# Kernel tuning notes

Hardware: AMD Instinct MI355X
Metric: run time of the kernel (lower is better)

Reference implementation:

```python
import jax, jax.numpy as jnp
import numpy as np

D_MODEL = 1024
N_HEADS = 16
D_HEAD = D_MODEL // N_HEADS
LORA_RANK = 8
LORA_ALPHA = 16
LORA_SCALING = LORA_ALPHA / LORA_RANK
NEG_INF = -1.0e9


def setup_inputs() -> dict:
    key = jax.random.key(0)
    ks = jax.random.split(key, 8)
    B, S = 2, 2048
    s_in = 1.0 / np.sqrt(D_MODEL)
    return {
        "x": jax.random.normal(ks[0], (B, S, D_MODEL), dtype=jnp.float32),
        "attention_mask": jnp.ones((B, S), dtype=jnp.int32),
        "W_qkv_kernel": jax.random.normal(ks[1], (D_MODEL, 3 * D_MODEL), jnp.float32) * s_in,
        "W_qkv_bias": jnp.zeros((3 * D_MODEL,), jnp.float32),
        "lora_A_qkv": jax.random.normal(ks[2], (D_MODEL, LORA_RANK), jnp.float32) * 0.01,
        "lora_B_qkv": jax.random.normal(ks[3], (LORA_RANK, 3 * D_MODEL), jnp.float32) * 0.01,
        "c_proj_kernel": jax.random.normal(ks[4], (D_MODEL, D_MODEL), jnp.float32) * s_in,
        "c_proj_bias": jnp.zeros((D_MODEL,), jnp.float32),
        "lora_A_proj": jax.random.normal(ks[5], (D_MODEL, LORA_RANK), jnp.float32) * 0.01,
        "lora_B_proj": jax.random.normal(ks[6], (LORA_RANK, D_MODEL), jnp.float32) * 0.01,
    }


def reference(x, attention_mask, W_qkv_kernel, W_qkv_bias, lora_A_qkv, lora_B_qkv,
              c_proj_kernel, c_proj_bias, lora_A_proj, lora_B_proj):
    B, S, _ = x.shape
    # QKV projection + LoRA adapter
    qkv = x @ W_qkv_kernel + W_qkv_bias
    qkv = qkv + ((x @ lora_A_qkv) @ lora_B_qkv) * LORA_SCALING
    q, k, v = jnp.split(qkv, 3, axis=-1)
    # [B, H, S, Dh]
    q = q.reshape(B, S, N_HEADS, D_HEAD).transpose(0, 2, 1, 3)
    k = k.reshape(B, S, N_HEADS, D_HEAD).transpose(0, 2, 1, 3)
    v = v.reshape(B, S, N_HEADS, D_HEAD).transpose(0, 2, 1, 3)
    # raw scores [B, H, S, S]
    scores = jnp.einsum("bhqd,bhkd->bhqk", q, k)
    # padding mask applied BEFORE scaling (as in the original)
    pad = (attention_mask[:, None, None, :] == 0)
    scores = jnp.where(pad, NEG_INF, scores)
    # causal mask (lower triangular kept)
    causal = jnp.tril(jnp.ones((S, S), dtype=bool))
    scores = jnp.where(causal[None, None, :, :], scores, NEG_INF)
    # scaling applied AFTER masking (faithful to source: -1e9 also divided)
    scaled = scores / jnp.sqrt(jnp.float32(D_HEAD))
    attn = jax.nn.softmax(scaled, axis=-1)
    ctx = jnp.einsum("bhqk,bhkd->bhqd", attn, v)
    ctx = ctx.transpose(0, 2, 1, 3).reshape(B, S, D_MODEL)
    out = ctx @ c_proj_kernel + c_proj_bias
    out = out + ((ctx @ lora_A_proj) @ lora_B_proj) * LORA_SCALING
    return out
```

## Files before the change

### kernel.cpp

```cpp
#include <hip/hip_runtime.h>
#include <hip/hip_bf16.h>

#define LOG2E 1.4426950408889634f
#define MASKVAL (-1.25e8f * LOG2E)

typedef __bf16 bf16x8 __attribute__((ext_vector_type(8)));
typedef __bf16 bf16x4 __attribute__((ext_vector_type(4)));
typedef short  shortx4 __attribute__((ext_vector_type(4)));
typedef float  floatx4 __attribute__((ext_vector_type(4)));

__device__ __forceinline__ floatx4 mfma16(bf16x8 a, bf16x8 b, floatx4 c) {
  return __builtin_amdgcn_mfma_f32_16x16x32_bf16(a, b, c, 0, 0, 0);
}

__device__ __forceinline__ floatx4 mfma_pv(bf16x4 a, bf16x4 b, floatx4 c) {
#if __has_builtin(__builtin_amdgcn_mfma_f32_16x16x16_bf16)
  return __builtin_amdgcn_mfma_f32_16x16x16_bf16(a, b, c, 0, 0, 0);
#else
  shortx4 as, bs;
  __builtin_memcpy(&as, &a, 8);
  __builtin_memcpy(&bs, &b, 8);
  return __builtin_amdgcn_mfma_f32_16x16x16bf16_1k(as, bs, c, 0, 0, 0);
#endif
}

__device__ __forceinline__ void load_lds16(const __bf16* g, __bf16* l) {
  __builtin_amdgcn_global_load_lds(
      (const __attribute__((address_space(1))) void*)g,
      (__attribute__((address_space(3))) void*)l, 16, 0, 0);
}

__device__ __forceinline__ float max3f(float a, float b, float c) {
  return fmaxf(a, fmaxf(b, c));
}

__global__ __launch_bounds__(256)
void fold_wt2(const float* __restrict__ Wq, const float* __restrict__ Aq,
              const float* __restrict__ Bq, __bf16* __restrict__ WTq,
              const float* __restrict__ Wp, const float* __restrict__ Ap,
              const float* __restrict__ Bp, __bf16* __restrict__ WTp) {
  __shared__ float tile[64][65];
  __shared__ float sLb[8][64];
  const int bx = blockIdx.x;
  const bool isQ = bx < 48;
  const float* W  = isQ ? Wq : Wp;
  const float* La = isQ ? Aq : Ap;
  const float* Lb = isQ ? Bq : Bp;
  __bf16* WT = isQ ? WTq : WTp;
  const int ncols = isQ ? 3072 : 1024;
  const int nt = (isQ ? bx : bx - 48) * 64;
  const int kt = blockIdx.y * 64;
  const int tid = threadIdx.x;
  const int tx = tid & 63, ty = tid >> 6;

  float rLa[8];
  *(float4*)&rLa[0] = *(const float4*)(La + (size_t)(kt + tx) * 8);
  *(float4*)&rLa[4] = *(const float4*)(La + (size_t)(kt + tx) * 8 + 4);

#pragma unroll
  for (int rep = 0; rep < 2; rep++) {
    int idx = tid + rep * 256;
    sLb[idx >> 6][idx & 63] = Lb[(size_t)(idx >> 6) * ncols + nt + (idx & 63)];
  }
#pragma unroll
  for (int rep = 0; rep < 16; rep++) {
    int i = rep * 4 + ty;
    tile[i][tx] = W[(size_t)(kt + i) * ncols + nt + tx];
  }
  __syncthreads();
#pragma unroll
  for (int rep = 0; rep < 16; rep++) {
    int i = rep * 4 + ty;
    int n = nt + i, k = kt + tx;
    float acc = tile[tx][i];
#pragma unroll
    for (int r = 0; r < 8; r++)
      acc += 2.0f * rLa[r] * sLb[r][i];
    WT[(size_t)n * 1024 + k] = (__bf16)acc;
  }
}

__global__ __launch_bounds__(256)
void cast_x(const float* __restrict__ x, __bf16* __restrict__ o) {
  int i = blockIdx.x * 256 + threadIdx.x;
  float4 v = ((const float4*)x)[i];
  bf16x4 r = {(__bf16)v.x, (__bf16)v.y, (__bf16)v.z, (__bf16)v.w};
  ((bf16x4*)o)[i] = r;
}

__global__ __launch_bounds__(256)
void gemm_qkv(const __bf16* __restrict__ WT, const __bf16* __restrict__ X,
              const float* __restrict__ bias, __bf16* __restrict__ qk,
              __bf16* __restrict__ vtb) {
  const int K = 1024;
  __shared__ alignas(16) __bf16 smem[32768];
  const int tid = threadIdx.x;
  const int wave = tid >> 6, lane = tid & 63;
  const int wm = wave >> 1, wn = wave & 1;
  const int quad = lane >> 4, l15 = lane & 15;
  const int p0 = blockIdx.y * 128, s0 = blockIdx.x * 128;
  const int srow8 = lane >> 3, sc8 = lane & 7;
  const int sswz = sc8 ^ srow8;

  auto STAGE = [&](int bb, int kb) {
    __bf16* Ab = smem + bb * 8192;
    __bf16* Bb = smem + 16384 + bb * 8192;
#pragma unroll
    for (int t = 0; t < 4; t++) {
      int rbase = (wave * 4 + t) * 8;
      int row = rbase + srow8;
      load_lds16(WT + (size_t)(p0 + row) * K + kb + sswz * 8, Ab + rbase * 64);
      load_lds16(X + (size_t)(s0 + row) * K + kb + sswz * 8, Bb + rbase * 64);
    }
  };

  floatx4 acc[4][4] = {};
  STAGE(0, 0);

  for (int it = 0; it < 16; it++) {
    const int cur = it & 1;
    if (it < 15) {
      STAGE(cur ^ 1, (it + 1) * 64);
      asm volatile("s_waitcnt vmcnt(8)" ::: "memory");
    } else {
      asm volatile("s_waitcnt vmcnt(0)" ::: "memory");
    }
    __builtin_amdgcn_s_barrier();
    __builtin_amdgcn_sched_barrier(0);
    const __bf16* Ac = smem + cur * 8192;
    const __bf16* Bc = smem + 16384 + cur * 8192;
#pragma unroll
    for (int ks = 0; ks < 2; ks++) {
      bf16x8 af[4], bfv[4];
#pragma unroll
      for (int t = 0; t < 4; t++) {
        int ra = wm * 64 + t * 16 + l15;
        int rb = wn * 64 + t * 16 + l15;
        int ch = (ks * 4 + quad) ^ (l15 & 7);
        af[t]  = *(const bf16x8*)(Ac + ra * 64 + ch * 8);
        bfv[t] = *(const bf16x8*)(Bc + rb * 64 + ch * 8);
      }
#pragma unroll
      for (int mi = 0; mi < 4; mi++)
#pragma unroll
        for (int ni = 0; ni < 4; ni++)
          acc[mi][ni] = mfma16(af[mi], bfv[ni], acc[mi][ni]);
    }
    __builtin_amdgcn_s_barrier();
  }

  __bf16* ep = smem;
  const int b = s0 >> 11, s2b = s0 & 2047;

  if (p0 < 2048) {
    const float qscale = (p0 < 1024) ? 0.125f * LOG2E : 1.0f;
#pragma unroll
    for (int mi = 0; mi < 4; mi++) {
      int ch0 = wm * 64 + mi * 16 + quad * 4;
      float4 b4 = *(const float4*)(bias + p0 + ch0);
#pragma unroll
      for (int ni = 0; ni < 4; ni++) {
        int tl = wn * 64 + ni * 16 + l15;
        bf16x4 o = {(__bf16)((acc[mi][ni][0] + b4.x) * qscale),
                    (__bf16)((acc[mi][ni][1] + b4.y) * qscale),
                    (__bf16)((acc[mi][ni][2] + b4.z) * qscale),
                    (__bf16)((acc[mi][ni][3] + b4.w) * qscale)};
        *(bf16x4*)(ep + tl * 136 + ch0) = o;
      }
    }
    __syncthreads();
    const int part = p0 >> 10;
    const int h0 = (p0 & 1023) >> 6;
    const int hs = wave & 1, tb = (wave >> 1) * 64;
    __bf16* outp = qk + (size_t)part * 4194304 +
                   ((size_t)((b * 16 + h0 + hs) * 2048 + s2b)) * 64;
#pragma unroll
    for (int j = 0; j < 8; j++) {
      int tok = tb + j * 8 + (lane >> 3);
      int dh = (lane & 7) * 8;
      bf16x8 v = *(const bf16x8*)(ep + tok * 136 + hs * 64 + dh);
      *(bf16x8*)(outp + (size_t)tok * 64 + dh) = v;
    }
  } else {
#pragma unroll
    for (int mi = 0; mi < 4; mi++) {
      int ch0 = wm * 64 + mi * 16 + quad * 4;
      float4 b4 = *(const float4*)(bias + p0 + ch0);
#pragma unroll
      for (int ni = 0; ni < 4; ni++) {
        int tl = wn * 64 + ni * 16 + l15;
        int off = tl & 63, t = off >> 4, qd = (off >> 2) & 3, rr = off & 3;
        int ptl = (tl & 64) | ((t >> 1) * 32 + qd * 8 + (t & 1) * 4 + rr);
        ep[(ch0 + 0) * 136 + ptl] = (__bf16)(acc[mi][ni][0] + b4.x);
        ep[(ch0 + 1) * 136 + ptl] = (__bf16)(acc[mi][ni][1] + b4.y);
        ep[(ch0 + 2) * 136 + ptl] = (__bf16)(acc[mi][ni][2] + b4.z);
        ep[(ch0 + 3) * 136 + ptl] = (__bf16)(acc[mi][ni][3] + b4.w);
      }
    }
    __syncthreads();
    const int h0 = (p0 & 1023) >> 6;
#pragma unroll
    for (int j = 0; j < 8; j++) {
      int ch = wave * 32 + j * 4 + (lane >> 4);
      int to = (lane & 15) * 8;
      bf16x8 v = *(const bf16x8*)(ep + ch * 136 + to);
      int h = h0 + (ch >> 6), dh = ch & 63;
      *(bf16x8*)(vtb + ((size_t)((b * 16 + h) * 64 + dh)) * 2048 + s2b + to) =
          v;
    }
  }
}

__global__ __launch_bounds__(256)
void gemm_proj(const __bf16* __restrict__ A, const __bf16* __restrict__ BT,
               const float* __restrict__ bias, float* __restrict__ Cout, int N) {
  const int K = 1024;
  __shared__ alignas(16) __bf16 smem[24576];
  const int tid = threadIdx.x;
  const int wave = tid >> 6, lane = tid & 63;
  const int wm = wave >> 1, wn = wave & 1;
  const int quad = lane >> 4, l15 = lane & 15;
  const int m0 = blockIdx.y * 64, n0 = blockIdx.x * 128;
  const int srow8 = lane >> 3, sc8 = lane & 7;
  const int sswz = sc8 ^ srow8;

  auto STAGE = [&](int bb, int kb) {
    __bf16* Ab = smem + bb * 4096;
    __bf16* Bb = smem + 8192 + bb * 8192;
#pragma unroll
    for (int t = 0; t < 2; t++) {
      int rbase = (wave * 2 + t) * 8;
      load_lds16(A + (size_t)(m0 + rbase + srow8) * K + kb + sswz * 8,
                 Ab + rbase * 64);
    }
#pragma unroll
    for (int t = 0; t < 4; t++) {
      int rbase = (wave * 4 + t) * 8;
      load_lds16(BT + (size_t)(n0 + rbase + srow8) * K + kb + sswz * 8,
                 Bb + rbase * 64);
    }
  };

  floatx4 acc[2][4] = {};
  STAGE(0, 0);

  for (int it = 0; it < 16; it++) {
    const int cur = it & 1;
    if (it < 15) {
      STAGE(cur ^ 1, (it + 1) * 64);
      asm volatile("s_waitcnt vmcnt(6)" ::: "memory");
    } else {
      asm volatile("s_waitcnt vmcnt(0)" ::: "memory");
    }
    __builtin_amdgcn_s_barrier();
    __builtin_amdgcn_sched_barrier(0);
    const __bf16* Ac = smem + cur * 4096;
    const __bf16* Bc = smem + 8192 + cur * 8192;
#pragma unroll
    for (int ks = 0; ks < 2; ks++) {
      bf16x8 af[2], bfv[4];
      int ch = (ks * 4 + quad) ^ (l15 & 7);
#pragma unroll
      for (int t = 0; t < 2; t++)
        af[t] = *(const bf16x8*)(Ac + (wm * 32 + t * 16 + l15) * 64 + ch * 8);
#pragma unroll
      for (int t = 0; t < 4; t++)
        bfv[t] = *(const bf16x8*)(Bc + (wn * 64 + t * 16 + l15) * 64 + ch * 8);
#pragma unroll
      for (int mi = 0; mi < 2; mi++)
#pragma unroll
        for (int ni = 0; ni < 4; ni++)
          acc[mi][ni] = mfma16(af[mi], bfv[ni], acc[mi][ni]);
    }
    __builtin_amdgcn_s_barrier();
  }

#pragma unroll
  for (int mi = 0; mi < 2; mi++)
#pragma unroll
    for (int ni = 0; ni < 4; ni++) {
      int n = n0 + wn * 64 + ni * 16 + l15;
#pragma unroll
      for (int r = 0; r < 4; r++) {
        int m = m0 + wm * 32 + mi * 16 + quad * 4 + r;
        Cout[(size_t)m * N + n] = acc[mi][ni][r] + bias[n];
      }
    }
}

__global__ __launch_bounds__(256)
void flash_attn(const __bf16* __restrict__ q, const __bf16* __restrict__ k,
                const __bf16* __restrict__ vt, const int* __restrict__ amask,
                __bf16* __restrict__ ctx) {
  const int S = 2048;
  __shared__ alignas(16) __bf16 Ks[2][64 * 64];
  __shared__ alignas(16) __bf16 Vs[2][64 * 64];
  const int bid = blockIdx.x;
  const int jb = 31 - (bid >> 5);
  const int bh = bid & 31;
  const int b = bh >> 4, h = bh & 15;
  const int wave = threadIdx.x >> 6, lane = threadIdx.x & 63;
  const int quad = lane >> 4, l15 = lane & 15;
  const int srow8 = lane >> 3, sc8 = lane & 7;
  const int sswz = sc8 ^ srow8;
  const int Q0 = jb * 64;
  const int qrow = Q0 + wave * 16 + l15;

  const __bf16* qp  = q  + (size_t)bh * S * 64;
  const __bf16* kp0 = k  + (size_t)bh * S * 64;
  const __bf16* vp0 = vt + (size_t)bh * 64 * S;

  int anyp = 0;
  const int npre = (jb + 4) >> 2;
  for (int it = 0; it < npre; it++) {
    int4 v = *(const int4*)(amask + b * S + it * 256 + lane * 4);
    anyp |= (v.x == 0) | (v.y == 0) | (v.z == 0) | (v.w == 0);
  }
  const bool padded = (__ballot(anyp) != 0ull);

  bf16x8 qf[2];
#pragma unroll
  for (int ks = 0; ks < 2; ks++)
    qf[ks] = *(const bf16x8*)(qp + (size_t)qrow * 64 + ks * 32 + quad * 8);

  auto STAGE = [&](int bb, int cc) {
#pragma unroll
    for (int t = 0; t < 2; t++) {
      int rbase = (wave * 2 + t) * 8;
      load_lds16(kp0 + (size_t)cc * 4096 + (size_t)(rbase + srow8) * 64 +
                     sswz * 8,
                 &Ks[bb][rbase * 64]);
    }
#pragma unroll
    for (int t = 0; t < 2; t++) {
      int rbase = (wave * 2 + t) * 8;
      load_lds16(vp0 + (size_t)(rbase + srow8) * S + cc * 64 + sswz * 8,
                 &Vs[bb][rbase * 64]);
    }
  };

  STAGE(0, 0);

  float mrun = 0.0f, lrun = 0.0f;
  floatx4 oacc[4] = {};

  for (int c = 0; c <= jb; c++) {
    const int cur = c & 1;
    if (c < jb) {
      STAGE(cur ^ 1, c + 1);
      asm volatile("s_waitcnt vmcnt(4)" ::: "memory");
    } else {
      asm volatile("s_waitcnt vmcnt(0)" ::: "memory");
    }
    __builtin_amdgcn_s_barrier();
    __builtin_amdgcn_sched_barrier(0);

    floatx4 st[4] = {};
    __builtin_amdgcn_s_setprio(1);
#pragma unroll
    for (int ks = 0; ks < 2; ks++) {
      const int ch = (ks * 4 + quad) ^ (l15 & 7);
      bf16x8 kf[4];
#pragma unroll
      for (int nt = 0; nt < 4; nt++)
        kf[nt] = *(const bf16x8*)(&Ks[cur][(nt * 16 + l15) * 64 + ch * 8]);
#pragma unroll
      for (int nt = 0; nt < 4; nt++)
        st[nt] = mfma16(kf[nt], qf[ks], st[nt]);
    }
    __builtin_amdgcn_s_setprio(0);

    if (padded) {
      int am_c = amask[b * S + c * 64 + lane];
      unsigned long long pm = __ballot(am_c == 0);
#pragma unroll
      for (int nt = 0; nt < 4; nt++) {
        int kl = nt * 16 + quad * 4;
#pragma unroll
        for (int r = 0; r < 4; r++) {
          bool pad = (pm >> (kl + r)) & 1ull;
          bool masked = pad || ((c == jb) && (kl + r > wave * 16 + l15));
          st[nt][r] = masked ? MASKVAL : st[nt][r];
        }
      }
    } else if (c == jb) {
#pragma unroll
      for (int nt = 0; nt < 4; nt++) {
        int kl = nt * 16 + quad * 4;
#pragma unroll
        for (int r = 0; r < 4; r++) {
          bool masked = kl + r > wave * 16 + l15;
          st[nt][r] = masked ? MASKVAL : st[nt][r];
        }
      }
    }

    float t0 = max3f(st[0][0], st[0][1], st[0][2]);
    float t1 = max3f(st[0][3], st[1][0], st[1][1]);
    float t2 = max3f(st[1][2], st[1][3], st[2][0]);
    float t3 = max3f(st[2][1], st[2][2], st[2][3]);
    float t4 = max3f(st[3][0], st[3][1], st[3][2]);
    float inm = fmaxf(max3f(t0, t1, t2), max3f(t3, t4, st[3][3]));
#pragma unroll
    for (int nt = 0; nt < 4; nt++)
#pragma unroll
      for (int r = 0; r < 4; r++)
        st[nt][r] = exp2f(st[nt][r] - mrun);
    float ssum = (((st[0][0] + st[0][1]) + (st[0][2] + st[0][3])) +
                  ((st[1][0] + st[1][1]) + (st[1][2] + st[1][3]))) +
                 (((st[2][0] + st[2][1]) + (st[2][2] + st[2][3])) +
                  ((st[3][0] + st[3][1]) + (st[3][2] + st[3][3])));
    if (!__all(inm - mrun <= 8.0f)) {
      float rm = fmaxf(inm, __shfl_xor(inm, 16, 64));
      rm = fmaxf(rm, __shfl_xor(rm, 32, 64));
      float mnew = fmaxf(mrun, rm);
      float al = exp2f(mrun - mnew);
      mrun = mnew;
      lrun *= al;
      ssum *= al;
#pragma unroll
      for (int nt = 0; nt < 4; nt++)
#pragma unroll
        for (int r = 0; r < 4; r++) st[nt][r] *= al;
#pragma unroll
      for (int nd = 0; nd < 4; nd++)
#pragma unroll
        for (int r = 0; r < 4; r++) oacc[nd][r] *= al;
    }
    lrun += ssum;

    bf16x4 pB[4];
#pragma unroll
    for (int nt = 0; nt < 4; nt++) {
      bf16x4 pk = {(__bf16)st[nt][0], (__bf16)st[nt][1],
                   (__bf16)st[nt][2], (__bf16)st[nt][3]};
      pB[nt] = pk;
    }

    __builtin_amdgcn_s_setprio(1);
#pragma unroll
    for (int tp = 0; tp < 2; tp++) {
      const int chv = (tp * 4 + quad) ^ (l15 & 7);
#pragma unroll
      for (int nd = 0; nd < 4; nd++) {
        bf16x8 v8 =
            *(const bf16x8*)(&Vs[cur][(nd * 16 + l15) * 64 + chv * 8]);
        bf16x4 vA0 = {v8[0], v8[1], v8[2], v8[3]};
        bf16x4 vA1 = {v8[4], v8[5], v8[6], v8[7]};
        oacc[nd] = mfma_pv(vA0, pB[2 * tp], oacc[nd]);
        oacc[nd] = mfma_pv(vA1, pB[2 * tp + 1], oacc[nd]);
      }
    }
    __builtin_amdgcn_s_setprio(0);

    __builtin_amdgcn_s_barrier();
  }

  lrun += __shfl_xor(lrun, 16, 64);
  lrun += __shfl_xor(lrun, 32, 64);

  const float linv = 1.0f / lrun;
#pragma unroll
  for (int nd = 0; nd < 4; nd++) {
    bf16x4 o = {(__bf16)(oacc[nd][0] * linv), (__bf16)(oacc[nd][1] * linv),
                (__bf16)(oacc[nd][2] * linv), (__bf16)(oacc[nd][3] * linv)};
    *(bf16x4*)(ctx + ((size_t)(b * 2048 + qrow)) * 1024 + h * 64 + nd * 16 +
               quad * 4) = o;
  }
}

extern "C" void kernel_launch(void* const* d_in, const int* in_sizes, int n_in,
                              void* d_out, int out_size, void* d_ws, size_t ws_size,
                              hipStream_t stream) {
  const float* x  = (const float*)d_in[0];
  const int*   am = (const int*)d_in[1];
  const float* Wq = (const float*)d_in[2];
  const float* bq = (const float*)d_in[3];
  const float* Aq = (const float*)d_in[4];
  const float* Bq = (const float*)d_in[5];
  const float* Wp = (const float*)d_in[6];
  const float* bp = (const float*)d_in[7];
  const float* Ap = (const float*)d_in[8];
  const float* Bp = (const float*)d_in[9];

  __bf16* wqkvT = (__bf16*)d_ws;
  __bf16* wpT   = wqkvT + (size_t)3072 * 1024;
  __bf16* xbf   = wpT   + (size_t)1024 * 1024;
  __bf16* qbuf  = xbf   + (size_t)4096 * 1024;
  __bf16* vtbuf = qbuf  + (size_t)2 * 4194304;
  __bf16* ctxb  = vtbuf + (size_t)4194304;

  fold_wt2<<<dim3(64, 16), 256, 0, stream>>>(Wq, Aq, Bq, wqkvT,
                                             Wp, Ap, Bp, wpT);
  cast_x<<<4096, 256, 0, stream>>>(x, xbf);

  gemm_qkv<<<dim3(32, 24), 256, 0, stream>>>(wqkvT, xbf, bq, qbuf, vtbuf);
  flash_attn<<<1024, 256, 0, stream>>>(qbuf, qbuf + 4194304, vtbuf, am, ctxb);
  gemm_proj<<<dim3(8, 64), 256, 0, stream>>>(ctxb, wpT, bp, (float*)d_out, 1024);
}
```

Before: 187.2 us.

## Retile output projection to 128x128 swapped-operand tiles; unroll attention loop by two

The output projection GEMM moves from 64x128 tiles to 128x128 tiles with the weight as the M operand and ctx as N. Each thread can then write contiguous float4 outputs with vectorized bias loads instead of scalar strided stores, and reuse per staged tile goes up, but the grid shrinks to 256 blocks and LDS use grows. Flash attention now calls the raw hardware exp2 builtin instead of exp2f. Its chunk loop is unrolled by two so the double-buffer index is a compile-time constant.

```diff
diff --git a/kernel.cpp b/kernel.cpp
--- a/kernel.cpp
+++ b/kernel.cpp
@@ -32,6 +32,10 @@
 
 __device__ __forceinline__ float max3f(float a, float b, float c) {
   return fmaxf(a, fmaxf(b, c));
+}
+
+__device__ __forceinline__ float exp2r(float x) {
+  return __builtin_amdgcn_exp2f(x);
 }
 
 __global__ __launch_bounds__(256)
@@ -212,62 +216,60 @@
 }
 
 __global__ __launch_bounds__(256)
-void gemm_proj(const __bf16* __restrict__ A, const __bf16* __restrict__ BT,
+void gemm_proj(const __bf16* __restrict__ Actx, const __bf16* __restrict__ BT,
                const float* __restrict__ bias, float* __restrict__ Cout, int N) {
   const int K = 1024;
-  __shared__ alignas(16) __bf16 smem[24576];
+  __shared__ alignas(16) __bf16 smem[32768];
   const int tid = threadIdx.x;
   const int wave = tid >> 6, lane = tid & 63;
   const int wm = wave >> 1, wn = wave & 1;
   const int quad = lane >> 4, l15 = lane & 15;
-  const int m0 = blockIdx.y * 64, n0 = blockIdx.x * 128;
+  const int p0 = blockIdx.y * 128;
+  const int s0 = blockIdx.x * 128;
   const int srow8 = lane >> 3, sc8 = lane & 7;
   const int sswz = sc8 ^ srow8;
 
   auto STAGE = [&](int bb, int kb) {
-    __bf16* Ab = smem + bb * 4096;
-    __bf16* Bb = smem + 8192 + bb * 8192;
-#pragma unroll
-    for (int t = 0; t < 2; t++) {
-      int rbase = (wave * 2 + t) * 8;
-      load_lds16(A + (size_t)(m0 + rbase + srow8) * K + kb + sswz * 8,
-                 Ab + rbase * 64);
-    }
+    __bf16* Ab = smem + bb * 8192;
+    __bf16* Bb = smem + 16384 + bb * 8192;
 #pragma unroll
     for (int t = 0; t < 4; t++) {
       int rbase = (wave * 4 + t) * 8;
-      load_lds16(BT + (size_t)(n0 + rbase + srow8) * K + kb + sswz * 8,
+      int row = rbase + srow8;
+      load_lds16(BT + (size_t)(p0 + row) * K + kb + sswz * 8, Ab + rbase * 64);
+      load_lds16(Actx + (size_t)(s0 + row) * K + kb + sswz * 8,
                  Bb + rbase * 64);
     }
   };
 
-  floatx4 acc[2][4] = {};
+  floatx4 acc[4][4] = {};
   STAGE(0, 0);
 
   for (int it = 0; it < 16; it++) {
     const int cur = it & 1;
     if (it < 15) {
       STAGE(cur ^ 1, (it + 1) * 64);
-      asm volatile("s_waitcnt vmcnt(6)" ::: "memory");
+      asm volatile("s_waitcnt vmcnt(8)" ::: "memory");
     } else {
       asm volatile("s_waitcnt vmcnt(0)" ::: "memory");
     }
     __builtin_amdgcn_s_barrier();
     __builtin_amdgcn_sched_barrier(0);
-    const __bf16* Ac = smem + cur * 4096;
-    const __bf16* Bc = smem + 8192 + cur * 8192;
+    const __bf16* Ac = smem + cur * 8192;
+    const __bf16* Bc = smem + 16384 + cur * 8192;
 #pragma unroll
     for (int ks = 0; ks < 2; ks++) {
-      bf16x8 af[2], bfv[4];
-      int ch = (ks * 4 + quad) ^ (l15 & 7);
-#pragma unroll
-      for (int t = 0; t < 2; t++)
-        af[t] = *(const bf16x8*)(Ac + (wm * 32 + t * 16 + l15) * 64 + ch * 8);
-#pragma unroll
-      for (int t = 0; t < 4; t++)
-        bfv[t] = *(const bf16x8*)(Bc + (wn * 64 + t * 16 + l15) * 64 + ch * 8);
-#pragma unroll
-      for (int mi = 0; mi < 2; mi++)
+      bf16x8 af[4], bfv[4];
+#pragma unroll
+      for (int t = 0; t < 4; t++) {
+        int ra = wm * 64 + t * 16 + l15;
+        int rb = wn * 64 + t * 16 + l15;
+        int ch = (ks * 4 + quad) ^ (l15 & 7);
+        af[t]  = *(const bf16x8*)(Ac + ra * 64 + ch * 8);
+        bfv[t] = *(const bf16x8*)(Bc + rb * 64 + ch * 8);
+      }
+#pragma unroll
+      for (int mi = 0; mi < 4; mi++)
 #pragma unroll
         for (int ni = 0; ni < 4; ni++)
           acc[mi][ni] = mfma16(af[mi], bfv[ni], acc[mi][ni]);
@@ -276,16 +278,17 @@
   }
 
 #pragma unroll
-  for (int mi = 0; mi < 2; mi++)
+  for (int mi = 0; mi < 4; mi++) {
+    int n = p0 + wm * 64 + mi * 16 + quad * 4;
+    float4 b4 = *(const float4*)(bias + n);
 #pragma unroll
     for (int ni = 0; ni < 4; ni++) {
-      int n = n0 + wn * 64 + ni * 16 + l15;
-#pragma unroll
-      for (int r = 0; r < 4; r++) {
-        int m = m0 + wm * 32 + mi * 16 + quad * 4 + r;
-        Cout[(size_t)m * N + n] = acc[mi][ni][r] + bias[n];
-      }
-    }
+      int m = s0 + wn * 64 + ni * 16 + l15;
+      float4 o = {acc[mi][ni][0] + b4.x, acc[mi][ni][1] + b4.y,
+                  acc[mi][ni][2] + b4.z, acc[mi][ni][3] + b4.w};
+      *(float4*)(Cout + (size_t)m * N + n) = o;
+    }
+  }
 }
 
 __global__ __launch_bounds__(256)
@@ -344,8 +347,7 @@
   float mrun = 0.0f, lrun = 0.0f;
   floatx4 oacc[4] = {};
 
-  for (int c = 0; c <= jb; c++) {
-    const int cur = c & 1;
+  auto CHUNK = [&](int c, int cur) {
     if (c < jb) {
       STAGE(cur ^ 1, c + 1);
       asm volatile("s_waitcnt vmcnt(4)" ::: "memory");
@@ -405,7 +407,7 @@
     for (int nt = 0; nt < 4; nt++)
 #pragma unroll
       for (int r = 0; r < 4; r++)
-        st[nt][r] = exp2f(st[nt][r] - mrun);
+        st[nt][r] = exp2r(st[nt][r] - mrun);
     float ssum = (((st[0][0] + st[0][1]) + (st[0][2] + st[0][3])) +
                   ((st[1][0] + st[1][1]) + (st[1][2] + st[1][3]))) +
                  (((st[2][0] + st[2][1]) + (st[2][2] + st[2][3])) +
@@ -414,7 +416,7 @@
       float rm = fmaxf(inm, __shfl_xor(inm, 16, 64));
       rm = fmaxf(rm, __shfl_xor(rm, 32, 64));
       float mnew = fmaxf(mrun, rm);
-      float al = exp2f(mrun - mnew);
+      float al = exp2r(mrun - mnew);
       mrun = mnew;
       lrun *= al;
       ssum *= al;
@@ -454,6 +456,11 @@
     __builtin_amdgcn_s_setprio(0);
 
     __builtin_amdgcn_s_barrier();
+  };
+
+  for (int c = 0; c <= jb; c += 2) {
+    CHUNK(c, 0);
+    if (c + 1 <= jb) CHUNK(c + 1, 1);
   }
 
   lrun += __shfl_xor(lrun, 16, 64);
@@ -496,5 +503,5 @@
 
   gemm_qkv<<<dim3(32, 24), 256, 0, stream>>>(wqkvT, xbf, bq, qbuf, vtbuf);
   flash_attn<<<1024, 256, 0, stream>>>(qbuf, qbuf + 4194304, vtbuf, am, ctxb);
-  gemm_proj<<<dim3(8, 64), 256, 0, stream>>>(ctxb, wpT, bp, (float*)d_out, 1024);
-}
+  gemm_proj<<<dim3(32, 8), 256, 0, stream>>>(ctxb, wpT, bp, (float*)d_out, 1024);
+}
```

After: 179.6 us. -4.1%, faster.

## Merge fold and cast kernels, transpose proj GEMM tiles, use raw exp2, unroll attention loop

Applied to the files above, without the earlier changes.

Merges the weight-fold and x-cast kernels into one launch, which removes a kernel launch. It swaps the operand roles in the output projection GEMM so each thread can write float4 stores with a vectorized bias load. The flash-attention loop is unrolled by two with a constant double-buffer index, and exp2f is replaced by the hardware exp2 intrinsic. The raw exp2 may differ slightly in denormal or accuracy handling.

```diff
diff --git a/kernel.cpp b/kernel.cpp
--- a/kernel.cpp
+++ b/kernel.cpp
@@ -34,14 +34,28 @@
   return fmaxf(a, fmaxf(b, c));
 }
 
+__device__ __forceinline__ float exp2r(float x) {
+  return __builtin_amdgcn_exp2f(x);
+}
+
 __global__ __launch_bounds__(256)
-void fold_wt2(const float* __restrict__ Wq, const float* __restrict__ Aq,
-              const float* __restrict__ Bq, __bf16* __restrict__ WTq,
-              const float* __restrict__ Wp, const float* __restrict__ Ap,
-              const float* __restrict__ Bp, __bf16* __restrict__ WTp) {
+void fold_cast(const float* __restrict__ Wq, const float* __restrict__ Aq,
+               const float* __restrict__ Bq, __bf16* __restrict__ WTq,
+               const float* __restrict__ Wp, const float* __restrict__ Ap,
+               const float* __restrict__ Bp, __bf16* __restrict__ WTp,
+               const float* __restrict__ x, __bf16* __restrict__ xo) {
+  const int bid = blockIdx.x;
+  const int tid = threadIdx.x;
+  if (bid >= 1024) {
+    int i = (bid - 1024) * 256 + tid;
+    float4 v = ((const float4*)x)[i];
+    bf16x4 r = {(__bf16)v.x, (__bf16)v.y, (__bf16)v.z, (__bf16)v.w};
+    ((bf16x4*)xo)[i] = r;
+    return;
+  }
   __shared__ float tile[64][65];
   __shared__ float sLb[8][64];
-  const int bx = blockIdx.x;
+  const int bx = bid & 63;
   const bool isQ = bx < 48;
   const float* W  = isQ ? Wq : Wp;
   const float* La = isQ ? Aq : Ap;
@@ -49,8 +63,7 @@
   __bf16* WT = isQ ? WTq : WTp;
   const int ncols = isQ ? 3072 : 1024;
   const int nt = (isQ ? bx : bx - 48) * 64;
-  const int kt = blockIdx.y * 64;
-  const int tid = threadIdx.x;
+  const int kt = (bid >> 6) * 64;
   const int tx = tid & 63, ty = tid >> 6;
 
   float rLa[8];
@@ -78,14 +91,6 @@
       acc += 2.0f * rLa[r] * sLb[r][i];
     WT[(size_t)n * 1024 + k] = (__bf16)acc;
   }
-}
-
-__global__ __launch_bounds__(256)
-void cast_x(const float* __restrict__ x, __bf16* __restrict__ o) {
-  int i = blockIdx.x * 256 + threadIdx.x;
-  float4 v = ((const float4*)x)[i];
-  bf16x4 r = {(__bf16)v.x, (__bf16)v.y, (__bf16)v.z, (__bf16)v.w};
-  ((bf16x4*)o)[i] = r;
 }
 
 __global__ __launch_bounds__(256)
@@ -212,7 +217,7 @@
 }
 
 __global__ __launch_bounds__(256)
-void gemm_proj(const __bf16* __restrict__ A, const __bf16* __restrict__ BT,
+void gemm_proj(const __bf16* __restrict__ Actx, const __bf16* __restrict__ BT,
                const float* __restrict__ bias, float* __restrict__ Cout, int N) {
   const int K = 1024;
   __shared__ alignas(16) __bf16 smem[24576];
@@ -220,7 +225,8 @@
   const int wave = tid >> 6, lane = tid & 63;
   const int wm = wave >> 1, wn = wave & 1;
   const int quad = lane >> 4, l15 = lane & 15;
-  const int m0 = blockIdx.y * 64, n0 = blockIdx.x * 128;
+  const int p0 = blockIdx.y * 64;
+  const int s0 = blockIdx.x * 128;
   const int srow8 = lane >> 3, sc8 = lane & 7;
   const int sswz = sc8 ^ srow8;
 
@@ -230,13 +236,13 @@
 #pragma unroll
     for (int t = 0; t < 2; t++) {
       int rbase = (wave * 2 + t) * 8;
-      load_lds16(A + (size_t)(m0 + rbase + srow8) * K + kb + sswz * 8,
+      load_lds16(BT + (size_t)(p0 + rbase + srow8) * K + kb + sswz * 8,
                  Ab + rbase * 64);
     }
 #pragma unroll
     for (int t = 0; t < 4; t++) {
       int rbase = (wave * 4 + t) * 8;
-      load_lds16(BT + (size_t)(n0 + rbase + srow8) * K + kb + sswz * 8,
+      load_lds16(Actx + (size_t)(s0 + rbase + srow8) * K + kb + sswz * 8,
                  Bb + rbase * 64);
     }
   };
@@ -276,16 +282,17 @@
   }
 
 #pragma unroll
-  for (int mi = 0; mi < 2; mi++)
+  for (int mi = 0; mi < 2; mi++) {
+    int n = p0 + wm * 32 + mi * 16 + quad * 4;
+    float4 b4 = *(const float4*)(bias + n);
 #pragma unroll
     for (int ni = 0; ni < 4; ni++) {
-      int n = n0 + wn * 64 + ni * 16 + l15;
-#pragma unroll
-      for (int r = 0; r < 4; r++) {
-        int m = m0 + wm * 32 + mi * 16 + quad * 4 + r;
-        Cout[(size_t)m * N + n] = acc[mi][ni][r] + bias[n];
-      }
-    }
+      int m = s0 + wn * 64 + ni * 16 + l15;
+      float4 o = {acc[mi][ni][0] + b4.x, acc[mi][ni][1] + b4.y,
+                  acc[mi][ni][2] + b4.z, acc[mi][ni][3] + b4.w};
+      *(float4*)(Cout + (size_t)m * N + n) = o;
+    }
+  }
 }
 
 __global__ __launch_bounds__(256)
@@ -344,8 +351,7 @@
   float mrun = 0.0f, lrun = 0.0f;
   floatx4 oacc[4] = {};
 
-  for (int c = 0; c <= jb; c++) {
-    const int cur = c & 1;
+  auto CHUNK = [&](int c, int cur) {
     if (c < jb) {
       STAGE(cur ^ 1, c + 1);
       asm volatile("s_waitcnt vmcnt(4)" ::: "memory");
@@ -405,7 +411,7 @@
     for (int nt = 0; nt < 4; nt++)
 #pragma unroll
       for (int r = 0; r < 4; r++)
-        st[nt][r] = exp2f(st[nt][r] - mrun);
+        st[nt][r] = exp2r(st[nt][r] - mrun);
     float ssum = (((st[0][0] + st[0][1]) + (st[0][2] + st[0][3])) +
                   ((st[1][0] + st[1][1]) + (st[1][2] + st[1][3]))) +
                  (((st[2][0] + st[2][1]) + (st[2][2] + st[2][3])) +
@@ -414,7 +420,7 @@
       float rm = fmaxf(inm, __shfl_xor(inm, 16, 64));
       rm = fmaxf(rm, __shfl_xor(rm, 32, 64));
       float mnew = fmaxf(mrun, rm);
-      float al = exp2f(mrun - mnew);
+      float al = exp2r(mrun - mnew);
       mrun = mnew;
       lrun *= al;
       ssum *= al;
@@ -454,6 +460,11 @@
     __builtin_amdgcn_s_setprio(0);
 
     __builtin_amdgcn_s_barrier();
+  };
+
+  for (int c = 0; c <= jb; c += 2) {
+    CHUNK(c, 0);
+    if (c + 1 <= jb) CHUNK(c + 1, 1);
   }
 
   lrun += __shfl_xor(lrun, 16, 64);
@@ -490,11 +501,10 @@
   __bf16* vtbuf = qbuf  + (size_t)2 * 4194304;
   __bf16* ctxb  = vtbuf + (size_t)4194304;
 
-  fold_wt2<<<dim3(64, 16), 256, 0, stream>>>(Wq, Aq, Bq, wqkvT,
-                                             Wp, Ap, Bp, wpT);
-  cast_x<<<4096, 256, 0, stream>>>(x, xbf);
+  fold_cast<<<5120, 256, 0, stream>>>(Wq, Aq, Bq, wqkvT, Wp, Ap, Bp, wpT,
+                                      x, xbf);
 
   gemm_qkv<<<dim3(32, 24), 256, 0, stream>>>(wqkvT, xbf, bq, qbuf, vtbuf);
   flash_attn<<<1024, 256, 0, stream>>>(qbuf, qbuf + 4194304, vtbuf, am, ctxb);
-  gemm_proj<<<dim3(8, 64), 256, 0, stream>>>(ctxb, wpT, bp, (float*)d_out, 1024);
-}
+  gemm_proj<<<dim3(32, 16), 256, 0, stream>>>(ctxb, wpT, bp, (float*)d_out, 1024);
+}
```

New measurement: 172.8 us, median of 2. 7.7% less time.
